# Kernel tuning notes

Measured on AMD Instinct MI355X. Metric: run time of the kernel, lower is better.

Reference implementation:

```python
import jax, jax.numpy as jnp
import numpy as np

STATE_DIM = 512
PROJ_DIM = 300


def setup_inputs() -> dict:
    key = jax.random.key(0)
    ks = jax.random.split(key, 10)
    batseq, node_num, edge_num = 320, 32, 1024  # edge_num = node_num**2
    inp = {
        "nodes_feats": jax.random.normal(ks[0], (batseq, node_num, STATE_DIM), jnp.float32),
        "edges_feats": jax.random.normal(ks[1], (batseq, edge_num, STATE_DIM), jnp.float32),
        "adj_mat": jax.random.uniform(ks[2], (batseq, node_num, edge_num), jnp.float32),
        "true_lengths": jax.random.randint(ks[3], (32,), 0, 10),
        "seq_size": 10,
        # Linear layer params (out_features=300, in_features=512), torch layout W: [out, in]
        "W1": jax.random.normal(ks[4], (PROJ_DIM, STATE_DIM), jnp.float32) * 0.02,
        "b1": jnp.zeros((PROJ_DIM,), jnp.float32),
        "W2": jax.random.normal(ks[5], (PROJ_DIM, STATE_DIM), jnp.float32) * 0.02,
        "b2": jnp.zeros((PROJ_DIM,), jnp.float32),
        "W3": jax.random.normal(ks[6], (PROJ_DIM, STATE_DIM), jnp.float32) * 0.02,
        "b3": jnp.zeros((PROJ_DIM,), jnp.float32),
    }
    return inp


def reference(nodes_feats, edges_feats, adj_mat, true_lengths, seq_size,
              W1, b1, W2, b2, W3, b3):
    batseq, node_num, _ = nodes_feats.shape
    batch = batseq // seq_size  # from adj_mat.view(-1, seq_size, node_num, edge_num)
    # Batched replacements for the per-pair tiny Linears
    f1 = jnp.einsum("bnd,pd->bnp", nodes_feats, W1) + b1   # [B, N, 300]
    f3 = jnp.einsum("bnd,pd->bnp", nodes_feats, W3) + b3   # [B, N, 300]
    f2 = jnp.einsum("bed,pd->bep", edges_feats, W2) + b2   # [B, N*N, 300]
    f2 = f2.reshape(batseq, node_num, node_num, PROJ_DIM)  # [B, i, j, 300]
    # per-pair MSE(f_j, f_ij + f_i), mean over (batseq, 300), summed over (i, j)
    diff = f3[:, None, :, :] - f2 - f1[:, :, None, :]
    losses = jnp.sum(diff * diff) / (batseq * PROJ_DIM)
    return losses / batch
```

## Files before the change

kernel.cpp:

```cpp
#include <hip/hip_runtime.h>
#include <hip/hip_bf16.h>
#include <stdint.h>

#define STATE 512
#define PROJ 300
#define PPAD 320
#define BATSEQ 320
#define TE 327680
#define PSTR 328

typedef __bf16 bf16x8 __attribute__((ext_vector_type(8)));
typedef float f32x4 __attribute__((ext_vector_type(4)));
typedef float f32x2 __attribute__((ext_vector_type(2)));
typedef long long i64;

__device__ inline unsigned short f2bf(float x) {
  unsigned u = __builtin_bit_cast(unsigned, x);
  unsigned r = u + 0x7fffu + ((u >> 16) & 1u);
  return (unsigned short)(r >> 16);
}

__global__ __launch_bounds__(256) void prep_kernel(
    const float* __restrict__ W1, const float* __restrict__ b1,
    const float* __restrict__ W2, const float* __restrict__ b2,
    const float* __restrict__ W3, const float* __restrict__ b3,
    unsigned short* __restrict__ w1p, unsigned short* __restrict__ w3p,
    unsigned short* __restrict__ w2tp, unsigned char* __restrict__ w2p8,
    float* __restrict__ b1p, float* __restrict__ b2p, float* __restrict__ b3p)
{
  int idx = blockIdx.x * 256 + threadIdx.x;
  const int WN = PPAD * STATE;
  if (idx < 2 * WN) {
    int which = idx / WN, r = idx % WN;
    int cs = r / 512, q = r % 512;
    int lane = q / 8, i = q % 8;
    int c = cs / 16, s = cs % 16;
    int p = c * 16 + (lane & 15);
    int k = s * 32 + (lane >> 4) * 8 + i;
    const float* W = (which == 0) ? W1 : W3;
    unsigned short* dst = (which == 0) ? w1p : w3p;
    float v = (p < PROJ) ? W[(size_t)p * STATE + k] : 0.0f;
    dst[r] = f2bf(v);
  } else if (idx < 3 * WN) {
    int r = idx - 2 * WN;
    int cs = r / 512, q = r % 512;
    int lane = q / 8, ii = q % 8;
    int ct = cs / 10, s2 = cs % 10;
    int p = s2 * 32 + (lane >> 4) * 8 + ii;
    int n = ct * 16 + (lane & 15);
    float v = (p < PROJ) ? W2[(size_t)p * STATE + n] : 0.0f;
    w2tp[r] = f2bf(v);
  } else if (idx < 4 * WN) {
    int r = idx - 3 * WN;
    int cs = r / 512, q = r % 512;
    int lane = q / 8, i = q % 8;
    int c = cs / 16, s = cs % 16;
    int p = c * 16 + (lane & 15);
    int k = s * 32 + (lane >> 4) * 8 + i;
    float v = (p < PROJ) ? W2[(size_t)p * STATE + k] : 0.0f;
    int pk = __builtin_amdgcn_cvt_pk_fp8_f32(v, 0.f, 0, 0);
    w2p8[r] = (unsigned char)(pk & 0xff);
  } else if (idx < 4 * WN + 3 * PPAD) {
    int r = idx - 4 * WN;
    int which = r / PPAD, p = r % PPAD;
    const float* B = (which == 0) ? b1 : ((which == 1) ? b2 : b3);
    float* dst = (which == 0) ? b1p : ((which == 1) ? b2p : b3p);
    dst[p] = (p < PROJ) ? B[p] : 0.0f;
  }
}

__global__ __launch_bounds__(256, 2) void node_kernel(
    const float* __restrict__ nodes,
    const unsigned short* __restrict__ w1p, const unsigned short* __restrict__ w3p,
    const unsigned short* __restrict__ w2tp,
    const float* __restrict__ b1p, const float* __restrict__ b2p,
    const float* __restrict__ b3p,
    float* __restrict__ g1t, float* __restrict__ g3t,
    double* __restrict__ pnode)
{
  __shared__ __align__(16) unsigned short tile[32 * 512];
  __shared__ __align__(16) unsigned short t2a[32 * PSTR];
  __shared__ __align__(16) unsigned short t2b[32 * PSTR];
  __shared__ float G1[PPAD], G3[PPAD];
  __shared__ double red[4];
  const int tid = threadIdx.x;
  const int wave = tid >> 6, lane = tid & 63;
  const int b = blockIdx.x;
  const float* src = nodes + (size_t)b * 32 * STATE;

  for (int t = tid; t < PPAD; t += 256) { G1[t] = 0.f; G3[t] = 0.f; }

  #pragma unroll
  for (int m = 0; m < 16; ++m) {
    int k = wave + 4 * m;
    int row = k >> 1;
    int fc = (k & 1) * 64 + lane;
    f32x4 v = *(const f32x4*)(src + row * STATE + fc * 4);
    unsigned lo = f2bf(v.x) | ((unsigned)f2bf(v.y) << 16);
    unsigned hi = f2bf(v.z) | ((unsigned)f2bf(v.w) << 16);
    unsigned long long pk = (unsigned long long)lo | ((unsigned long long)hi << 32);
    unsigned off = (unsigned)(row * 1024 + fc * 8) ^ (unsigned)((row & 7) << 4);
    *(unsigned long long*)((char*)tile + off) = pk;
  }
  __syncthreads();

  const int lrow = lane & 15, lk = lane >> 4;
  const int cbase = wave * 5;

  f32x4 af1[2][5], af3[2][5];
  #pragma unroll
  for (int rg = 0; rg < 2; ++rg)
    #pragma unroll
    for (int c = 0; c < 5; ++c) {
      af1[rg][c][0]=0.f; af1[rg][c][1]=0.f; af1[rg][c][2]=0.f; af1[rg][c][3]=0.f;
      af3[rg][c][0]=0.f; af3[rg][c][1]=0.f; af3[rg][c][2]=0.f; af3[rg][c][3]=0.f;
    }
  for (int s = 0; s < 16; ++s) {
    bf16x8 a[2];
    #pragma unroll
    for (int rg = 0; rg < 2; ++rg) {
      int row = rg * 16 + lrow;
      unsigned off = (unsigned)(row * 1024 + s * 64 + lk * 16) ^ (unsigned)((row & 7) << 4);
      a[rg] = *(const bf16x8*)((const char*)tile + off);
    }
    #pragma unroll
    for (int c = 0; c < 5; ++c) {
      size_t fo = ((size_t)(((cbase + c) * 16 + s) * 64 + lane)) * 8;
      bf16x8 bf1 = *(const bf16x8*)(w1p + fo);
      bf16x8 bf3 = *(const bf16x8*)(w3p + fo);
      #pragma unroll
      for (int rg = 0; rg < 2; ++rg) {
        af1[rg][c] = __builtin_amdgcn_mfma_f32_16x16x32_bf16(a[rg], bf1, af1[rg][c], 0, 0, 0);
        af3[rg][c] = __builtin_amdgcn_mfma_f32_16x16x32_bf16(a[rg], bf3, af3[rg][c], 0, 0, 0);
      }
    }
  }

  float sq = 0.f;
  #pragma unroll
  for (int rg = 0; rg < 2; ++rg)
    #pragma unroll
    for (int c = 0; c < 5; ++c) {
      int p = (cbase + c) * 16 + lrow;
      float bb1 = b1p[p], bb2 = b2p[p], bb3 = b3p[p];
      #pragma unroll
      for (int r = 0; r < 4; ++r) {
        int m = rg * 16 + lk * 4 + r;
        float v1 = af1[rg][c][r] + bb1;
        float v3 = af3[rg][c][r] + bb3 - bb2;
        t2a[m * PSTR + p] = f2bf(v1);
        t2b[m * PSTR + p] = f2bf(v3);
        sq += v1 * v1 + v3 * v3;
        atomicAdd(&G1[p], v1);
        atomicAdd(&G3[p], v3);
      }
    }
  __syncthreads();

  float s7 = 0.f;
  for (int t = tid; t < PPAD; t += 256) s7 += G3[t] * G1[t];
  float val = 32.f * sq - 2.f * s7;
  #pragma unroll
  for (int m = 32; m >= 1; m >>= 1) val += __shfl_xor(val, m, 64);
  if (lane == 0) red[wave] = (double)val;

  for (int pass = 0; pass < 2; ++pass) {
    const unsigned short* t2 = pass ? t2b : t2a;
    float* gt = pass ? g3t : g1t;
    f32x4 acc2[2][8];
    #pragma unroll
    for (int rg = 0; rg < 2; ++rg)
      #pragma unroll
      for (int cc = 0; cc < 8; ++cc) { acc2[rg][cc][0]=0.f; acc2[rg][cc][1]=0.f; acc2[rg][cc][2]=0.f; acc2[rg][cc][3]=0.f; }
    for (int s2 = 0; s2 < 10; ++s2) {
      bf16x8 a[2];
      #pragma unroll
      for (int rg = 0; rg < 2; ++rg) {
        int mrow = rg * 16 + lrow;
        a[rg] = *(const bf16x8*)(t2 + mrow * PSTR + s2 * 32 + lk * 8);
      }
      #pragma unroll
      for (int cc = 0; cc < 8; ++cc) {
        int ct = wave * 8 + cc;
        bf16x8 bfr = *(const bf16x8*)(w2tp + ((size_t)((ct * 10 + s2) * 64 + lane)) * 8);
        #pragma unroll
        for (int rg = 0; rg < 2; ++rg)
          acc2[rg][cc] = __builtin_amdgcn_mfma_f32_16x16x32_bf16(a[rg], bfr, acc2[rg][cc], 0, 0, 0);
      }
    }
    #pragma unroll
    for (int rg = 0; rg < 2; ++rg)
      #pragma unroll
      for (int cc = 0; cc < 8; ++cc) {
        int n = (wave * 8 + cc) * 16 + lrow;
        #pragma unroll
        for (int r = 0; r < 4; ++r) {
          int mm = rg * 16 + lk * 4 + r;
          gt[((size_t)b * 32 + mm) * STATE + n] = acc2[rg][cc][r];
        }
      }
  }

  __syncthreads();
  if (tid == 0) pnode[b] = red[0] + red[1] + red[2] + red[3];
}

__global__ __launch_bounds__(256, 4) void edge_kernel(
    const float* __restrict__ edges, const unsigned char* __restrict__ w2p8,
    const float* __restrict__ g1t, const float* __restrict__ g3t,
    double* __restrict__ pedge)
{
  __shared__ __align__(16) unsigned char tile[64 * 512];
  __shared__ double redd[4][2];
  const int tid = threadIdx.x;
  const int wave = tid >> 6, lane = tid & 63;

  const int orig = blockIdx.x;
  const int wg = (orig & 7) * 640 + (orig >> 3);
  const int b = wg >> 4, q = wg & 15;
  const float* src = edges + ((size_t)b * 1024 + (size_t)q * 64) * STATE;
  const float* g3b = g3t + (size_t)b * 32 * STATE;
  const float* g1b = g1t + ((size_t)b * 32 + (size_t)q * 2) * STATE;

  float cr = 0.f;
  f32x4 sE0 = {0.f, 0.f, 0.f, 0.f}, sE1 = {0.f, 0.f, 0.f, 0.f};
  const int fc = tid & 127;
  const int rhi = tid >> 7;
  #pragma unroll 16
  for (int m = 0; m < 32; ++m) {
    int row = 2 * m + rhi;
    f32x4 e = *(const f32x4*)(src + row * STATE + fc * 4);
    if (m < 16) sE0 += e; else sE1 += e;
    int pk = __builtin_amdgcn_cvt_pk_fp8_f32(e.x, e.y, 0, 0);
    pk = __builtin_amdgcn_cvt_pk_fp8_f32(e.z, e.w, pk, 1);
    unsigned off = (unsigned)(row * 512 + fc * 4) ^ (unsigned)((row & 7) << 3);
    *(int*)(tile + off) = pk;
  }
  {
    f32x4 g1a = *(const f32x4*)(g1b + fc * 4);
    f32x4 g1c = *(const f32x4*)(g1b + STATE + fc * 4);
    cr -= sE0.x * g1a.x + sE0.y * g1a.y + sE0.z * g1a.z + sE0.w * g1a.w;
    cr -= sE1.x * g1c.x + sE1.y * g1c.y + sE1.z * g1c.z + sE1.w * g1c.w;
  }
  __syncthreads();

  const int lrow = lane & 15, lk = lane >> 4;
  const int cb = wave * 5;
  f32x4 acc[4][5];
  #pragma unroll
  for (int rg = 0; rg < 4; ++rg)
    #pragma unroll
    for (int c = 0; c < 5; ++c) { acc[rg][c][0]=0.f; acc[rg][c][1]=0.f; acc[rg][c][2]=0.f; acc[rg][c][3]=0.f; }
  for (int s = 0; s < 16; ++s) {
    i64 a[4];
    #pragma unroll
    for (int rg = 0; rg < 4; ++rg) {
      int row = rg * 16 + lrow;
      unsigned off = (unsigned)(row * 512 + s * 32 + lk * 8) ^ (unsigned)((row & 7) << 3);
      a[rg] = *(const i64*)(tile + off);
    }
    #pragma unroll
    for (int c = 0; c < 5; ++c) {
      i64 bfr = *(const i64*)(w2p8 + ((size_t)(((cb + c) * 16 + s) * 64 + lane)) * 8);
      #pragma unroll
      for (int rg = 0; rg < 4; ++rg)
        acc[rg][c] = __builtin_amdgcn_mfma_f32_16x16x32_fp8_fp8(a[rg], bfr, acc[rg][c], 0, 0, 0);
    }
  }

  float ss = 0.f;
  #pragma unroll
  for (int rg = 0; rg < 4; ++rg)
    #pragma unroll
    for (int c = 0; c < 5; ++c)
      #pragma unroll
      for (int r = 0; r < 4; ++r) ss += acc[rg][c][r] * acc[rg][c][r];

  {
    const int j = tid >> 3, s8 = tid & 7;
    const float* g3r = g3b + (size_t)j * STATE + s8 * 64;
    const unsigned sw = (unsigned)((j & 7) << 3);
    float part = 0.f;
    #pragma unroll
    for (int c = 0; c < 8; ++c) {
      unsigned o0 = (unsigned)(j * 512 + s8 * 64 + c * 8) ^ sw;
      unsigned o1 = (unsigned)((j + 32) * 512 + s8 * 64 + c * 8) ^ sw;
      i64 p0 = *(const i64*)(tile + o0);
      i64 p1 = *(const i64*)(tile + o1);
      int l0 = (int)(p0 & 0xffffffffll), h0 = (int)(((unsigned long long)p0) >> 32);
      int l1 = (int)(p1 & 0xffffffffll), h1 = (int)(((unsigned long long)p1) >> 32);
      f32x2 a0 = __builtin_amdgcn_cvt_pk_f32_fp8(l0, 0);
      f32x2 a1 = __builtin_amdgcn_cvt_pk_f32_fp8(l0, 1);
      f32x2 a2 = __builtin_amdgcn_cvt_pk_f32_fp8(h0, 0);
      f32x2 a3 = __builtin_amdgcn_cvt_pk_f32_fp8(h0, 1);
      f32x2 c0 = __builtin_amdgcn_cvt_pk_f32_fp8(l1, 0);
      f32x2 c1 = __builtin_amdgcn_cvt_pk_f32_fp8(l1, 1);
      f32x2 c2 = __builtin_amdgcn_cvt_pk_f32_fp8(h1, 0);
      f32x2 c3 = __builtin_amdgcn_cvt_pk_f32_fp8(h1, 1);
      f32x4 g0 = *(const f32x4*)(g3r + c * 8);
      f32x4 g1v = *(const f32x4*)(g3r + c * 8 + 4);
      part += (a0.x + c0.x) * g0.x + (a0.y + c0.y) * g0.y
            + (a1.x + c1.x) * g0.z + (a1.y + c1.y) * g0.w
            + (a2.x + c2.x) * g1v.x + (a2.y + c2.y) * g1v.y
            + (a3.x + c3.x) * g1v.z + (a3.y + c3.y) * g1v.w;
    }
    cr += part;
  }

  #pragma unroll
  for (int m = 32; m >= 1; m >>= 1) {
    ss += __shfl_xor(ss, m, 64);
    cr += __shfl_xor(cr, m, 64);
  }
  if (lane == 0) { redd[wave][0] = (double)ss; redd[wave][1] = (double)cr; }
  __syncthreads();
  if (tid == 0) {
    double sT = 0.0, cT = 0.0;
    #pragma unroll
    for (int w = 0; w < 4; ++w) { sT += redd[w][0]; cT += redd[w][1]; }
    pedge[wg] = sT - 2.0 * cT;
  }
}

__global__ __launch_bounds__(256) void final_kernel(
    const double* __restrict__ pedge, const double* __restrict__ pnode,
    const int* __restrict__ seqp, float* __restrict__ out)
{
  __shared__ double red[4];
  const int tid = threadIdx.x, wave = tid >> 6, lane = tid & 63;
  double v = 0.0;
  for (int t = tid; t < 5120; t += 256) v += pedge[t];
  for (int t = tid; t < 320; t += 256) v += pnode[t];
  #pragma unroll
  for (int m = 32; m >= 1; m >>= 1) v += __shfl_xor(v, m, 64);
  if (lane == 0) red[wave] = v;
  __syncthreads();
  if (tid == 0) {
    double Total = red[0] + red[1] + red[2] + red[3];
    int seq = seqp[0];
    int batch = (seq > 0) ? (BATSEQ / seq) : 1;
    out[0] = (float)(Total / ((double)BATSEQ * (double)PROJ) / (double)batch);
  }
}

extern "C" void kernel_launch(void* const* d_in, const int* in_sizes, int n_in,
                              void* d_out, int out_size, void* d_ws, size_t ws_size,
                              hipStream_t stream)
{
  const float* nodes = (const float*)d_in[0];
  const float* edges = (const float*)d_in[1];
  const int*   seqp  = (const int*)d_in[4];
  const float* W1 = (const float*)d_in[5];
  const float* b1 = (const float*)d_in[6];
  const float* W2 = (const float*)d_in[7];
  const float* b2 = (const float*)d_in[8];
  const float* W3 = (const float*)d_in[9];
  const float* b3 = (const float*)d_in[10];

  char* ws = (char*)d_ws;
  unsigned short* w1p  = (unsigned short*)(ws + 0);
  unsigned short* w3p  = (unsigned short*)(ws + 327680);
  unsigned short* w2tp = (unsigned short*)(ws + 655360);
  unsigned char*  w2p8 = (unsigned char*)(ws + 983040);
  float* b1p = (float*)(ws + 1146880);
  float* b2p = (float*)(ws + 1148160);
  float* b3p = (float*)(ws + 1149440);
  float* g1t = (float*)(ws + 2097152);
  float* g3t = (float*)(ws + 23068672);
  double* pedge = (double*)(ws + 44040192);
  double* pnode = (double*)(ws + 44081152);

  prep_kernel<<<2564, 256, 0, stream>>>(W1, b1, W2, b2, W3, b3,
                                        w1p, w3p, w2tp, w2p8, b1p, b2p, b3p);
  node_kernel<<<320, 256, 0, stream>>>(nodes, w1p, w3p, w2tp, b1p, b2p, b3p,
                                       g1t, g3t, pnode);
  edge_kernel<<<5120, 256, 0, stream>>>(edges, w2p8, g1t, g3t, pedge);
  final_kernel<<<1, 256, 0, stream>>>(pedge, pnode, seqp, (float*)d_out);
}
```

Measured before the change: 350.6 us.

## Warp-specialize edge kernel into producer/consumer waves with double-buffered LDS tiles

```diff
diff --git a/kernel.cpp b/kernel.cpp
--- a/kernel.cpp
+++ b/kernel.cpp
@@ -8,6 +8,7 @@
 #define BATSEQ 320
 #define TE 327680
 #define PSTR 328
+#define TPB 10
 
 typedef __bf16 bf16x8 __attribute__((ext_vector_type(8)));
 typedef float f32x4 __attribute__((ext_vector_type(4)));
@@ -205,120 +206,136 @@
   if (tid == 0) pnode[b] = red[0] + red[1] + red[2] + red[3];
 }
 
-__global__ __launch_bounds__(256, 4) void edge_kernel(
+__global__ __launch_bounds__(512, 4) void edge_kernel(
     const float* __restrict__ edges, const unsigned char* __restrict__ w2p8,
     const float* __restrict__ g1t, const float* __restrict__ g3t,
     double* __restrict__ pedge)
 {
-  __shared__ __align__(16) unsigned char tile[64 * 512];
-  __shared__ double redd[4][2];
+  __shared__ __align__(16) unsigned char bufs[2][64 * 512];
+  __shared__ double redd[8][2];
   const int tid = threadIdx.x;
   const int wave = tid >> 6, lane = tid & 63;
 
   const int orig = blockIdx.x;
-  const int wg = (orig & 7) * 640 + (orig >> 3);
-  const int b = wg >> 4, q = wg & 15;
-  const float* src = edges + ((size_t)b * 1024 + (size_t)q * 64) * STATE;
-  const float* g3b = g3t + (size_t)b * 32 * STATE;
-  const float* g1b = g1t + ((size_t)b * 32 + (size_t)q * 2) * STATE;
-
-  float cr = 0.f;
-  f32x4 sE0 = {0.f, 0.f, 0.f, 0.f}, sE1 = {0.f, 0.f, 0.f, 0.f};
-  const int fc = tid & 127;
-  const int rhi = tid >> 7;
-  #pragma unroll 16
-  for (int m = 0; m < 32; ++m) {
-    int row = 2 * m + rhi;
-    f32x4 e = *(const f32x4*)(src + row * STATE + fc * 4);
-    if (m < 16) sE0 += e; else sE1 += e;
-    int pk = __builtin_amdgcn_cvt_pk_fp8_f32(e.x, e.y, 0, 0);
-    pk = __builtin_amdgcn_cvt_pk_fp8_f32(e.z, e.w, pk, 1);
-    unsigned off = (unsigned)(row * 512 + fc * 4) ^ (unsigned)((row & 7) << 3);
-    *(int*)(tile + off) = pk;
-  }
-  {
-    f32x4 g1a = *(const f32x4*)(g1b + fc * 4);
-    f32x4 g1c = *(const f32x4*)(g1b + STATE + fc * 4);
-    cr -= sE0.x * g1a.x + sE0.y * g1a.y + sE0.z * g1a.z + sE0.w * g1a.w;
-    cr -= sE1.x * g1c.x + sE1.y * g1c.y + sE1.z * g1c.z + sE1.w * g1c.w;
-  }
-  __syncthreads();
-
-  const int lrow = lane & 15, lk = lane >> 4;
-  const int cb = wave * 5;
-  f32x4 acc[4][5];
-  #pragma unroll
-  for (int rg = 0; rg < 4; ++rg)
-    #pragma unroll
-    for (int c = 0; c < 5; ++c) { acc[rg][c][0]=0.f; acc[rg][c][1]=0.f; acc[rg][c][2]=0.f; acc[rg][c][3]=0.f; }
-  for (int s = 0; s < 16; ++s) {
-    i64 a[4];
-    #pragma unroll
-    for (int rg = 0; rg < 4; ++rg) {
-      int row = rg * 16 + lrow;
-      unsigned off = (unsigned)(row * 512 + s * 32 + lk * 8) ^ (unsigned)((row & 7) << 3);
-      a[rg] = *(const i64*)(tile + off);
-    }
-    #pragma unroll
-    for (int c = 0; c < 5; ++c) {
-      i64 bfr = *(const i64*)(w2p8 + ((size_t)(((cb + c) * 16 + s) * 64 + lane)) * 8);
+  const int wg0 = (orig & 7) * 640 + (orig >> 3) * TPB;
+
+  if (wave < 4) {
+    const int fc = tid & 127;
+    const int rhi = tid >> 7;
+    float crp = 0.f;
+    for (int r = 0; r < TPB; ++r) {
+      const int wg = wg0 + r;
+      const int b = wg >> 4, q = wg & 15;
+      const float* src = edges + ((size_t)b * 1024 + (size_t)q * 64) * STATE;
+      const float* g1b = g1t + ((size_t)b * 32 + (size_t)q * 2) * STATE;
+      unsigned char* buf = &bufs[r & 1][0];
+      f32x4 sE0 = {0.f,0.f,0.f,0.f}, sE1 = {0.f,0.f,0.f,0.f};
+      #pragma unroll 8
+      for (int m = 0; m < 32; ++m) {
+        int row = 2 * m + rhi;
+        f32x4 e = *(const f32x4*)(src + row * STATE + fc * 4);
+        if (m < 16) sE0 += e; else sE1 += e;
+        int pk = __builtin_amdgcn_cvt_pk_fp8_f32(e.x, e.y, 0, 0);
+        pk = __builtin_amdgcn_cvt_pk_fp8_f32(e.z, e.w, pk, 1);
+        unsigned off = (unsigned)(row * 512 + fc * 4) ^ (unsigned)((row & 7) << 3);
+        *(int*)(buf + off) = pk;
+      }
+      f32x4 g1a = *(const f32x4*)(g1b + fc * 4);
+      f32x4 g1c = *(const f32x4*)(g1b + STATE + fc * 4);
+      crp -= sE0.x * g1a.x + sE0.y * g1a.y + sE0.z * g1a.z + sE0.w * g1a.w;
+      crp -= sE1.x * g1c.x + sE1.y * g1c.y + sE1.z * g1c.z + sE1.w * g1c.w;
+      __syncthreads();
+    }
+    #pragma unroll
+    for (int m = 32; m >= 1; m >>= 1) crp += __shfl_xor(crp, m, 64);
+    if (lane == 0) { redd[wave][0] = 0.0; redd[wave][1] = (double)crp; }
+  } else {
+    const int wid = wave - 4;
+    const int lrow = lane & 15, lk = lane >> 4;
+    const int cb = wid * 5;
+    const int tc = tid - 256;
+    float ssT = 0.f, crT = 0.f;
+    __syncthreads();
+    for (int r = 0; r < TPB; ++r) {
+      const unsigned char* buf = &bufs[r & 1][0];
+      const int wg = wg0 + r;
+      const int b = wg >> 4;
+      const float* g3b = g3t + (size_t)b * 32 * STATE;
+
+      f32x4 acc[4][5];
       #pragma unroll
       for (int rg = 0; rg < 4; ++rg)
-        acc[rg][c] = __builtin_amdgcn_mfma_f32_16x16x32_fp8_fp8(a[rg], bfr, acc[rg][c], 0, 0, 0);
-    }
-  }
-
-  float ss = 0.f;
-  #pragma unroll
-  for (int rg = 0; rg < 4; ++rg)
-    #pragma unroll
-    for (int c = 0; c < 5; ++c)
-      #pragma unroll
-      for (int r = 0; r < 4; ++r) ss += acc[rg][c][r] * acc[rg][c][r];
-
-  {
-    const int j = tid >> 3, s8 = tid & 7;
-    const float* g3r = g3b + (size_t)j * STATE + s8 * 64;
-    const unsigned sw = (unsigned)((j & 7) << 3);
-    float part = 0.f;
-    #pragma unroll
-    for (int c = 0; c < 8; ++c) {
-      unsigned o0 = (unsigned)(j * 512 + s8 * 64 + c * 8) ^ sw;
-      unsigned o1 = (unsigned)((j + 32) * 512 + s8 * 64 + c * 8) ^ sw;
-      i64 p0 = *(const i64*)(tile + o0);
-      i64 p1 = *(const i64*)(tile + o1);
-      int l0 = (int)(p0 & 0xffffffffll), h0 = (int)(((unsigned long long)p0) >> 32);
-      int l1 = (int)(p1 & 0xffffffffll), h1 = (int)(((unsigned long long)p1) >> 32);
-      f32x2 a0 = __builtin_amdgcn_cvt_pk_f32_fp8(l0, 0);
-      f32x2 a1 = __builtin_amdgcn_cvt_pk_f32_fp8(l0, 1);
-      f32x2 a2 = __builtin_amdgcn_cvt_pk_f32_fp8(h0, 0);
-      f32x2 a3 = __builtin_amdgcn_cvt_pk_f32_fp8(h0, 1);
-      f32x2 c0 = __builtin_amdgcn_cvt_pk_f32_fp8(l1, 0);
-      f32x2 c1 = __builtin_amdgcn_cvt_pk_f32_fp8(l1, 1);
-      f32x2 c2 = __builtin_amdgcn_cvt_pk_f32_fp8(h1, 0);
-      f32x2 c3 = __builtin_amdgcn_cvt_pk_f32_fp8(h1, 1);
-      f32x4 g0 = *(const f32x4*)(g3r + c * 8);
-      f32x4 g1v = *(const f32x4*)(g3r + c * 8 + 4);
-      part += (a0.x + c0.x) * g0.x + (a0.y + c0.y) * g0.y
-            + (a1.x + c1.x) * g0.z + (a1.y + c1.y) * g0.w
-            + (a2.x + c2.x) * g1v.x + (a2.y + c2.y) * g1v.y
-            + (a3.x + c3.x) * g1v.z + (a3.y + c3.y) * g1v.w;
-    }
-    cr += part;
-  }
-
-  #pragma unroll
-  for (int m = 32; m >= 1; m >>= 1) {
-    ss += __shfl_xor(ss, m, 64);
-    cr += __shfl_xor(cr, m, 64);
-  }
-  if (lane == 0) { redd[wave][0] = (double)ss; redd[wave][1] = (double)cr; }
+        #pragma unroll
+        for (int c = 0; c < 5; ++c) { acc[rg][c][0]=0.f; acc[rg][c][1]=0.f; acc[rg][c][2]=0.f; acc[rg][c][3]=0.f; }
+      for (int s = 0; s < 16; ++s) {
+        i64 a[4];
+        #pragma unroll
+        for (int rg = 0; rg < 4; ++rg) {
+          int row = rg * 16 + lrow;
+          unsigned off = (unsigned)(row * 512 + s * 32 + lk * 8) ^ (unsigned)((row & 7) << 3);
+          a[rg] = *(const i64*)(buf + off);
+        }
+        #pragma unroll
+        for (int c = 0; c < 5; ++c) {
+          i64 bfr = *(const i64*)(w2p8 + ((size_t)(((cb + c) * 16 + s) * 64 + lane)) * 8);
+          #pragma unroll
+          for (int rg = 0; rg < 4; ++rg)
+            acc[rg][c] = __builtin_amdgcn_mfma_f32_16x16x32_fp8_fp8(a[rg], bfr, acc[rg][c], 0, 0, 0);
+        }
+      }
+      #pragma unroll
+      for (int rg = 0; rg < 4; ++rg)
+        #pragma unroll
+        for (int c = 0; c < 5; ++c)
+          #pragma unroll
+          for (int rr = 0; rr < 4; ++rr) ssT += acc[rg][c][rr] * acc[rg][c][rr];
+
+      {
+        const int j = tc >> 3, s8 = tc & 7;
+        const float* g3r = g3b + (size_t)j * STATE + s8 * 64;
+        const unsigned sw = (unsigned)((j & 7) << 3);
+        float part = 0.f;
+        #pragma unroll
+        for (int c = 0; c < 8; ++c) {
+          unsigned o0 = (unsigned)(j * 512 + s8 * 64 + c * 8) ^ sw;
+          unsigned o1 = (unsigned)((j + 32) * 512 + s8 * 64 + c * 8) ^ sw;
+          i64 p0 = *(const i64*)(buf + o0);
+          i64 p1 = *(const i64*)(buf + o1);
+          int l0 = (int)(p0 & 0xffffffffll), h0 = (int)(((unsigned long long)p0) >> 32);
+          int l1 = (int)(p1 & 0xffffffffll), h1 = (int)(((unsigned long long)p1) >> 32);
+          f32x2 a0 = __builtin_amdgcn_cvt_pk_f32_fp8(l0, 0);
+          f32x2 a1 = __builtin_amdgcn_cvt_pk_f32_fp8(l0, 1);
+          f32x2 a2 = __builtin_amdgcn_cvt_pk_f32_fp8(h0, 0);
+          f32x2 a3 = __builtin_amdgcn_cvt_pk_f32_fp8(h0, 1);
+          f32x2 c0 = __builtin_amdgcn_cvt_pk_f32_fp8(l1, 0);
+          f32x2 c1 = __builtin_amdgcn_cvt_pk_f32_fp8(l1, 1);
+          f32x2 c2 = __builtin_amdgcn_cvt_pk_f32_fp8(h1, 0);
+          f32x2 c3 = __builtin_amdgcn_cvt_pk_f32_fp8(h1, 1);
+          f32x4 g0 = *(const f32x4*)(g3r + c * 8);
+          f32x4 g1v = *(const f32x4*)(g3r + c * 8 + 4);
+          part += (a0.x + c0.x) * g0.x + (a0.y + c0.y) * g0.y
+                + (a1.x + c1.x) * g0.z + (a1.y + c1.y) * g0.w
+                + (a2.x + c2.x) * g1v.x + (a2.y + c2.y) * g1v.y
+                + (a3.x + c3.x) * g1v.z + (a3.y + c3.y) * g1v.w;
+        }
+        crT += part;
+      }
+      if (r < TPB - 1) __syncthreads();
+    }
+    #pragma unroll
+    for (int m = 32; m >= 1; m >>= 1) {
+      ssT += __shfl_xor(ssT, m, 64);
+      crT += __shfl_xor(crT, m, 64);
+    }
+    if (lane == 0) { redd[wave][0] = (double)ssT; redd[wave][1] = (double)crT; }
+  }
+
   __syncthreads();
   if (tid == 0) {
     double sT = 0.0, cT = 0.0;
     #pragma unroll
-    for (int w = 0; w < 4; ++w) { sT += redd[w][0]; cT += redd[w][1]; }
-    pedge[wg] = sT - 2.0 * cT;
+    for (int w = 0; w < 8; ++w) { sT += redd[w][0]; cT += redd[w][1]; }
+    pedge[orig] = sT - 2.0 * cT;
   }
 }
 
@@ -329,7 +346,7 @@
   __shared__ double red[4];
   const int tid = threadIdx.x, wave = tid >> 6, lane = tid & 63;
   double v = 0.0;
-  for (int t = tid; t < 5120; t += 256) v += pedge[t];
+  for (int t = tid; t < 512; t += 256) v += pedge[t];
   for (int t = tid; t < 320; t += 256) v += pnode[t];
   #pragma unroll
   for (int m = 32; m >= 1; m >>= 1) v += __shfl_xor(v, m, 64);
@@ -368,12 +385,12 @@
   float* g1t = (float*)(ws + 2097152);
   float* g3t = (float*)(ws + 23068672);
   double* pedge = (double*)(ws + 44040192);
-  double* pnode = (double*)(ws + 44081152);
+  double* pnode = (double*)(ws + 44048384);
 
   prep_kernel<<<2564, 256, 0, stream>>>(W1, b1, W2, b2, W3, b3,
                                         w1p, w3p, w2tp, w2p8, b1p, b2p, b3p);
   node_kernel<<<320, 256, 0, stream>>>(nodes, w1p, w3p, w2tp, b1p, b2p, b3p,
                                        g1t, g3t, pnode);
-  edge_kernel<<<5120, 256, 0, stream>>>(edges, w2p8, g1t, g3t, pedge);
+  edge_kernel<<<512, 512, 0, stream>>>(edges, w2p8, g1t, g3t, pedge);
   final_kernel<<<1, 256, 0, stream>>>(pedge, pnode, seqp, (float*)d_out);
 }
```

Measured after the change: 661.1 us. +88.6%, slower.
